# Kernel optimization log

Measured on AMD Instinct MI355X. Metric: run time of the kernel, lower is better.

Reference implementation:

```python
import jax, jax.numpy as jnp
import numpy as np

H = 8          # n_heads
M = 16         # max_dist
U = 512        # n_units
DH = U // H    # d_head
EPS = 1e-3     # keras LayerNormalization default epsilon
NEG = -2.0**32 + 1.0


def _rel_table(pe, T):
    # pe: [2M+1, DH]; returns [T, T, DH] with rel[i, j] = pe[clip(j - i, -M, M) + M]
    i = jnp.arange(T)
    idx = jnp.clip(i[None, :] - i[:, None], -M, M) + M
    return pe[idx]


def _split_heads(x):
    # [B, T, U] -> [H*B, T, DH]  (head-major, matching tf.concat(tf.split(x, H, 2), 0))
    B, T, _ = x.shape
    return x.reshape(B, T, H, DH).transpose(2, 0, 1, 3).reshape(H * B, T, DH)


def _merge_heads(x, B):
    # [H*B, T, DH] -> [B, T, U]
    T = x.shape[1]
    return x.reshape(H, B, T, DH).transpose(1, 2, 0, 3).reshape(B, T, U)


def setup_inputs() -> dict:
    key = jax.random.key(0)
    ks = jax.random.split(key, 10)
    B, T = 8, 1024
    s = 1.0 / np.sqrt(U)
    inp = {
        'q': jax.random.normal(ks[0], (B, T, U), jnp.float32),
        'k': jax.random.normal(ks[1], (B, T, U), jnp.float32),
        'v': jax.random.normal(ks[2], (B, T, U), jnp.float32),
        'Wq': jax.random.normal(ks[3], (U, U), jnp.float32) * s,
        'bq': jnp.zeros((U,), jnp.float32),
        'Wk': jax.random.normal(ks[4], (U, U), jnp.float32) * s,
        'bk': jnp.zeros((U,), jnp.float32),
        'Wv': jax.random.normal(ks[5], (U, U), jnp.float32) * s,
        'bv': jnp.zeros((U,), jnp.float32),
        'Wo': jax.random.normal(ks[6], (U, U), jnp.float32) * s,
        'bo': jnp.zeros((U,), jnp.float32),
        'gamma': jnp.ones((U,), jnp.float32),
        'beta': jnp.zeros((U,), jnp.float32),
        'pe_k': jax.random.normal(ks[7], (2 * M + 1, DH), jnp.float32) * 0.05,
        'pe_v': jax.random.normal(ks[8], (2 * M + 1, DH), jnp.float32) * 0.05,
    }
    return inp


def reference(q, k, v, Wq, bq, Wk, bk, Wv, bv, Wo, bo, gamma, beta, pe_k, pe_v):
    B, T, _ = q.shape
    relu = jax.nn.relu
    q_emb = relu(q @ Wq + bq)
    k_emb = relu(k @ Wk + bk)
    v_emb = relu(v @ Wv + bv)
    qh = _split_heads(q_emb)   # [HB, T, DH]
    kh = _split_heads(k_emb)
    vh = _split_heads(v_emb)

    attn = jnp.einsum('btd,bsd->bts', qh, kh)
    rel_k = _rel_table(pe_k, T)                       # [T, T, DH]
    attn = attn + jnp.einsum('btd,tsd->bts', qh, rel_k)
    attn = attn / jnp.asarray(DH, attn.dtype) ** 0.5

    causal = jnp.tril(jnp.ones((T, T), jnp.bool_))
    attn = jnp.where(causal[None], attn, jnp.asarray(NEG, attn.dtype))
    w = jax.nn.softmax(attn, axis=-1)

    out = jnp.einsum('bts,bsd->btd', w, vh)
    rel_v = _rel_table(pe_v, T)
    out = out + jnp.einsum('bts,tsd->btd', w, rel_v)

    out = _merge_heads(out, B)                        # [B, T, U]
    out = relu(out @ Wo + bo)
    out = out + q

    mu = jnp.mean(out, axis=-1, keepdims=True)
    var = jnp.mean(jnp.square(out - mu), axis=-1, keepdims=True)
    return (out - mu) * jax.lax.rsqrt(var + EPS) * gamma + beta
```

## Files before the change

### kernel.cpp

```cpp
#include <hip/hip_runtime.h>
#include <hip/hip_bf16.h>

#define T_SEQ 1024
#define U_DIM 512
#define LN_EPS 1e-3f
#define LOG2E 1.44269504f

typedef float  f32x4  __attribute__((ext_vector_type(4)));
typedef short  bf16x8 __attribute__((ext_vector_type(8)));

__device__ __forceinline__ unsigned short f2bf(float f) {
    union { float f; unsigned u; } x; x.f = f;
    unsigned r = x.u + 0x7fffu + ((x.u >> 16) & 1u);
    return (unsigned short)(r >> 16);
}
__device__ __forceinline__ float b2f(short s) {
    union { unsigned u; float f; } x; x.u = ((unsigned)(unsigned short)s) << 16;
    return x.f;
}
__device__ __forceinline__ int packbf(float a, float b) {
    return (int)((unsigned)f2bf(a) | ((unsigned)f2bf(b) << 16));
}
__device__ __forceinline__ void async_copy16(void* lds, const void* g) {
    __builtin_amdgcn_global_load_lds((const __attribute__((address_space(1))) void*)g,
                                     (__attribute__((address_space(3))) void*)lds, 16, 0, 0);
}

#define WAITV(N) asm volatile("s_waitcnt vmcnt(" #N ")" ::: "memory")

__global__ __launch_bounds__(256) void prep_wt(
        const float* __restrict__ Wq, const float* __restrict__ Wk,
        const float* __restrict__ Wv, const float* __restrict__ Wo,
        short* __restrict__ wt) {
    __shared__ float Ws[64][65];
    const int bid = blockIdx.x, t = threadIdx.x;
    const int z = bid >> 6, tile = bid & 63;
    const float* W = (z == 0) ? Wq : (z == 1) ? Wk : (z == 2) ? Wv : Wo;
    short* Wt = wt + (size_t)z * 262144;
    const int k0 = (tile >> 3) * 64, n0 = (tile & 7) * 64;
    {
        const int kr = t >> 2, cs = (t & 3) * 16;
        const float4* src = (const float4*)(W + (size_t)(k0 + kr) * 512 + n0 + cs);
#pragma unroll
        for (int i = 0; i < 4; ++i) {
            float4 vv = src[i];
            Ws[kr][cs + 4 * i + 0] = vv.x;
            Ws[kr][cs + 4 * i + 1] = vv.y;
            Ws[kr][cs + 4 * i + 2] = vv.z;
            Ws[kr][cs + 4 * i + 3] = vv.w;
        }
    }
    __syncthreads();
    {
        const int nr = t >> 2, ks = (t & 3) * 16;
        int4 w0, w1;
        w0.x = packbf(Ws[ks + 0][nr], Ws[ks + 1][nr]);
        w0.y = packbf(Ws[ks + 2][nr], Ws[ks + 3][nr]);
        w0.z = packbf(Ws[ks + 4][nr], Ws[ks + 5][nr]);
        w0.w = packbf(Ws[ks + 6][nr], Ws[ks + 7][nr]);
        w1.x = packbf(Ws[ks + 8][nr], Ws[ks + 9][nr]);
        w1.y = packbf(Ws[ks + 10][nr], Ws[ks + 11][nr]);
        w1.z = packbf(Ws[ks + 12][nr], Ws[ks + 13][nr]);
        w1.w = packbf(Ws[ks + 14][nr], Ws[ks + 15][nr]);
        short* dst = Wt + (size_t)(n0 + nr) * 512 + k0 + ks;
        *(int4*)dst = w0;
        *(int4*)(dst + 8) = w1;
    }
}

__global__ __launch_bounds__(256) void gemm_cvt(
        const float* __restrict__ A0, const float* __restrict__ A1, const float* __restrict__ A2,
        const short* __restrict__ Wt0, const short* __restrict__ Wt1, const short* __restrict__ Wt2,
        const float* __restrict__ b0p, const float* __restrict__ b1p, const float* __restrict__ b2p,
        short* __restrict__ O0, short* __restrict__ O1, short* __restrict__ O2) {
    __shared__ short As[2 * 8192];
    __shared__ short Bs[2 * 8192];

    const int z = blockIdx.z;
    const float* Av = (z == 0) ? A0 : (z == 1) ? A1 : A2;
    const short* Wz = (z == 0) ? Wt0 : (z == 1) ? Wt1 : Wt2;
    const float* bz = (z == 0) ? b0p : (z == 1) ? b1p : b2p;
    short* Ov = (z == 0) ? O0 : (z == 1) ? O1 : O2;

    const int tid = threadIdx.x;
    const int m0 = blockIdx.x * 128, n0 = blockIdx.y * 128;
    const int w = tid >> 6, lane = tid & 63;
    const int n15 = lane & 15, g = lane >> 4;
    const int mh = w >> 1, nh = w & 1;
    const int lr = tid >> 4, c4 = tid & 15;

    f32x4 acc[4][4];
#pragma unroll
    for (int i = 0; i < 4; ++i)
#pragma unroll
        for (int j = 0; j < 4; ++j) acc[i][j] = (f32x4){0.f, 0.f, 0.f, 0.f};

    float4 areg[8];

#define LOAD_A(CK)                                                                       \
    do {                                                                                 \
        const float* abase = Av + (size_t)(m0 + lr) * 512 + (CK) * 64 + c4 * 4;          \
        _Pragma("unroll")                                                                \
        for (int i = 0; i < 8; ++i) areg[i] = *(const float4*)(abase + (size_t)8192 * i); \
    } while (0)

#define STORE_A(BUF)                                                                     \
    do {                                                                                 \
        short* sb = As + (BUF) * 8192 + (c4 >> 3) * 8 * 512 + lr * 8 +                   \
                    ((c4 & 7) >> 1) * 128 + (c4 & 1) * 4;                                \
        _Pragma("unroll")                                                                \
        for (int i = 0; i < 8; ++i) {                                                    \
            int2 wv;                                                                     \
            wv.x = packbf(areg[i].x, areg[i].y);                                         \
            wv.y = packbf(areg[i].z, areg[i].w);                                         \
            *(int2*)(sb + i * 512) = wv;                                                 \
        }                                                                                \
    } while (0)

#define STAGE_B(CK, BUF)                                                                 \
    do {                                                                                 \
        if (w < 2) {                                                                     \
            _Pragma("unroll")                                                            \
            for (int i = 0; i < 8; ++i) {                                                \
                const int kc = i >> 2, nt = w * 4 + (i & 3);                             \
                const short* gp = Wz + (size_t)(n0 + nt * 16 + n15) * 512 + (CK) * 64 + kc * 32 + g * 8; \
                async_copy16(Bs + (BUF) * 8192 + (kc * 8 + nt) * 512, gp);               \
            }                                                                            \
        }                                                                                \
    } while (0)

    LOAD_A(0);
    STORE_A(0);
    STAGE_B(0, 0);
    LOAD_A(1);

    for (int ck = 0; ck < 8; ++ck) {
        const int cb = ck & 1, nb = cb ^ 1;
        __syncthreads();
        if (ck < 7) STAGE_B(ck + 1, nb);
#pragma unroll
        for (int kc = 0; kc < 2; ++kc) {
            bf16x8 af[4], bfv[4];
#pragma unroll
            for (int i = 0; i < 4; ++i)
                af[i] = *(const bf16x8*)(As + cb * 8192 + (kc * 8 + mh * 4 + i) * 512 + lane * 8);
#pragma unroll
            for (int j = 0; j < 4; ++j)
                bfv[j] = *(const bf16x8*)(Bs + cb * 8192 + (kc * 8 + nh * 4 + j) * 512 + lane * 8);
#pragma unroll
            for (int i = 0; i < 4; ++i)
#pragma unroll
                for (int j = 0; j < 4; ++j)
                    acc[i][j] = __builtin_amdgcn_mfma_f32_16x16x32_bf16(af[i], bfv[j], acc[i][j], 0, 0, 0);
        }
        if (ck < 7) {
            STORE_A(nb);
            if (ck < 6) LOAD_A(ck + 2);
        }
    }
#undef LOAD_A
#undef STORE_A
#undef STAGE_B

    const int mbase = m0 + mh * 64 + g * 4;
    const int nbase = n0 + nh * 64 + n15;
    const bool even = (n15 & 1) == 0;
    float bj[4];
#pragma unroll
    for (int j = 0; j < 4; ++j) bj[j] = bz[nbase + j * 16];

#pragma unroll
    for (int i = 0; i < 4; ++i) {
        const int mrow = mbase + i * 16;
#pragma unroll
        for (int j = 0; j < 4; ++j) {
            const int ncol = nbase + j * 16;
            f32x4 a = acc[i][j];
            float v0 = fmaxf(a[0] + bj[j], 0.f);
            float v1 = fmaxf(a[1] + bj[j], 0.f);
            float v2 = fmaxf(a[2] + bj[j], 0.f);
            float v3 = fmaxf(a[3] + bj[j], 0.f);
            unsigned t01 = (unsigned)packbf(v0, v1);
            unsigned t23 = (unsigned)packbf(v2, v3);
            unsigned x01 = (unsigned)__shfl_xor((int)t01, 1, 64);
            unsigned x23 = (unsigned)__shfl_xor((int)t23, 1, 64);
            if (even) {
                unsigned d0 = (t01 & 0xffffu) | (x01 << 16);
                unsigned d1 = (t01 >> 16) | (x01 & 0xffff0000u);
                *(unsigned*)(Ov + (size_t)(mrow + 0) * 512 + ncol) = d0;
                *(unsigned*)(Ov + (size_t)(mrow + 1) * 512 + ncol) = d1;
            } else {
                unsigned d2 = (x23 & 0xffffu) | (t23 << 16);
                unsigned d3 = (x23 >> 16) | (t23 & 0xffff0000u);
                *(unsigned*)(Ov + (size_t)(mrow + 2) * 512 + ncol - 1) = d2;
                *(unsigned*)(Ov + (size_t)(mrow + 3) * 512 + ncol - 1) = d3;
            }
        }
    }
}

template <int BM, int BN>
__global__ __launch_bounds__(256) void gemm_pipe(
        const short* __restrict__ Ab, const short* __restrict__ Wz,
        const float* __restrict__ bz, const float* __restrict__ resid,
        float* __restrict__ Oz) {
    constexpr int ASZ = BM * 32;
    constexpr int BSZ = BN * 32;
    constexpr int TSZ = ASZ + BSZ;
    constexpr int NA  = BM / 16;
    constexpr int NB  = BN / 16;
    constexpr int MW  = BM / 64;
    constexpr int NW  = 4 / MW;
    constexpr int AJ  = BN / (16 * NW);
    constexpr int LPW = (NA + NB) / 4;
    static_assert((NA + NB) % 4 == 0, "cells divisible by waves");
    __shared__ short Ls[4 * TSZ];

    const int tid = threadIdx.x;
    const int m0 = blockIdx.x * BM, n0 = blockIdx.y * BN;
    const int w = tid >> 6, lane = tid & 63;
    const int n15 = lane & 15, g = lane >> 4;
    const int mh = w / NW, nh = w % NW;

    f32x4 acc[4][AJ];
#pragma unroll
    for (int i = 0; i < 4; ++i)
#pragma unroll
        for (int j = 0; j < AJ; ++j) acc[i][j] = (f32x4){0.f, 0.f, 0.f, 0.f};

    const short* gsrc[LPW];
    int loff[LPW];
#pragma unroll
    for (int cl = 0; cl < LPW; ++cl) {
        const int cid = w * LPW + cl;
        if (cid < NA) {
            gsrc[cl] = Ab + (size_t)(m0 + cid * 16 + n15) * 512 + g * 8;
            loff[cl] = cid * 512;
        } else {
            const int c2 = cid - NA;
            gsrc[cl] = Wz + (size_t)(n0 + c2 * 16 + n15) * 512 + g * 8;
            loff[cl] = ASZ + c2 * 512;
        }
    }

#define STAGE(CK, BUF)                                                                   \
    do {                                                                                 \
        _Pragma("unroll")                                                                \
        for (int cl = 0; cl < LPW; ++cl)                                                 \
            async_copy16(Ls + (BUF) * TSZ + loff[cl], gsrc[cl] + (CK) * 32);             \
    } while (0)

    STAGE(0, 0);
    STAGE(1, 1);
    STAGE(2, 2);

    for (int ck = 0; ck < 16; ++ck) {
        if (ck < 14) {
            if constexpr (LPW == 3) WAITV(6); else WAITV(4);
        } else if (ck == 14) {
            if constexpr (LPW == 3) WAITV(3); else WAITV(2);
        } else {
            WAITV(0);
        }
        __builtin_amdgcn_s_barrier();
        __builtin_amdgcn_sched_barrier(0);
        if (ck + 3 <= 15) STAGE(ck + 3, (ck + 3) & 3);
        const int cb = ck & 3;
        bf16x8 af[4], bfv[AJ];
#pragma unroll
        for (int i = 0; i < 4; ++i)
            af[i] = *(const bf16x8*)(Ls + cb * TSZ + (mh * 4 + i) * 512 + lane * 8);
#pragma unroll
        for (int j = 0; j < AJ; ++j)
            bfv[j] = *(const bf16x8*)(Ls + cb * TSZ + ASZ + (nh * AJ + j) * 512 + lane * 8);
#pragma unroll
        for (int i = 0; i < 4; ++i)
#pragma unroll
            for (int j = 0; j < AJ; ++j)
                acc[i][j] = __builtin_amdgcn_mfma_f32_16x16x32_bf16(af[i], bfv[j], acc[i][j], 0, 0, 0);
    }
#undef STAGE

    const int mbase = m0 + mh * 64 + g * 4;
    const int nbase = n0 + nh * (AJ * 16) + n15;
    const bool even = (n15 & 1) == 0;
    float bj[AJ];
#pragma unroll
    for (int j = 0; j < AJ; ++j) bj[j] = bz[nbase + j * 16];

#pragma unroll
    for (int i = 0; i < 4; ++i) {
        const int mrow = mbase + i * 16;
#pragma unroll
        for (int j = 0; j < AJ; ++j) {
            const int ncol = nbase + j * 16;
            f32x4 a = acc[i][j];
            float v0 = fmaxf(a[0] + bj[j], 0.f);
            float v1 = fmaxf(a[1] + bj[j], 0.f);
            float v2 = fmaxf(a[2] + bj[j], 0.f);
            float v3 = fmaxf(a[3] + bj[j], 0.f);
            float x0 = __shfl_xor(v0, 1, 64);
            float x1 = __shfl_xor(v1, 1, 64);
            float x2 = __shfl_xor(v2, 1, 64);
            float x3 = __shfl_xor(v3, 1, 64);
            if (even) {
                float2 r0 = *(const float2*)(resid + (size_t)(mrow + 0) * 512 + ncol);
                float2 r1 = *(const float2*)(resid + (size_t)(mrow + 1) * 512 + ncol);
                *(float2*)(Oz + (size_t)(mrow + 0) * 512 + ncol) = make_float2(v0 + r0.x, x0 + r0.y);
                *(float2*)(Oz + (size_t)(mrow + 1) * 512 + ncol) = make_float2(v1 + r1.x, x1 + r1.y);
            } else {
                float2 r2 = *(const float2*)(resid + (size_t)(mrow + 2) * 512 + ncol - 1);
                float2 r3 = *(const float2*)(resid + (size_t)(mrow + 3) * 512 + ncol - 1);
                *(float2*)(Oz + (size_t)(mrow + 2) * 512 + ncol - 1) = make_float2(x2 + r2.x, v2 + r2.y);
                *(float2*)(Oz + (size_t)(mrow + 3) * 512 + ncol - 1) = make_float2(x3 + r3.x, v3 + r3.y);
            }
        }
    }
}

__global__ __launch_bounds__(256, 4) void attn_mfma(
        const short* __restrict__ qe, const short* __restrict__ ke,
        const short* __restrict__ ve, const float* __restrict__ pe_k,
        float* __restrict__ ml, float* __restrict__ ml1, float* __restrict__ ml2,
        short* __restrict__ ao, short* __restrict__ ao2) {
    __shared__ short Kc[4096];
    __shared__ short Vc[4096];
    __shared__ float qpeS[4 * 16 * 17];

    static const unsigned char tbl[24] = {
        7, 22, 6, 4, 3, 1,
        20, 23, 16, 12, 9, 0,
        18, 5, 14, 15, 17, 2,
        19, 21, 8, 10, 11, 13
    };

    const int tid = threadIdx.x;
    const int r6 = blockIdx.x >> 8, c = blockIdx.x & 255;
    const int hb = c >> 2, q4 = c & 3;
    const int slot = tbl[q4 * 6 + r6];
    int tt, g0, g1, mode;
    if (slot < 8) {
        tt = slot; g0 = 0; g1 = slot + 1; mode = 0;
    } else {
        const int i2 = (slot - 8) >> 1;
        tt = 8 + i2;
        const int n = tt + 1, hh = (n + 1) >> 1;
        if (((slot - 8) & 1) == 0) { g0 = 0; g1 = hh; mode = 1; }
        else                       { g0 = hh; g1 = n; mode = 2; }
    }
    const int h = hb >> 3, b = hb & 7;
    const int w = tid >> 6, lane = tid & 63;
    const int g = lane >> 4, n15 = lane & 15;
    const int sp = tid & 31, dbase = (tid >> 5) * 8;
    float* qpeW = qpeS + w * (16 * 17);

    const size_t rowbase = (size_t)b * T_SEQ;
    short* aoP = (mode == 2) ? ao2 : ao;
    float* mlP = (mode == 0) ? ml : (mode == 1 ? ml1 : ml2);

    const int qn = tt * 64 + w * 16;
    bf16x8 Bq[2];
    float qpe0 = 0.f;
    float m_r = -1.0e38f, l_r = 0.f, m2 = -1.4427e38f;
    f32x4 oacc[4];

    {
#pragma unroll
        for (int kh = 0; kh < 2; ++kh) {
            bf16x8 t = *(const bf16x8*)(qe + (rowbase + qn + n15) * U_DIM + h * 64 + kh * 32 + g * 8);
#pragma unroll
            for (int i2 = 0; i2 < 8; ++i2) {
                unsigned short u = (unsigned short)t[i2];
                t[i2] = (short)(((u & 0x7f80u) > 0x0180u) ? (unsigned short)(u - 0x0180u)
                                                          : (unsigned short)(u & 0x8000u));
            }
            Bq[kh] = t;
        }
        f32x4 qa[2];
        qa[0] = (f32x4){0.f, 0.f, 0.f, 0.f};
        qa[1] = (f32x4){0.f, 0.f, 0.f, 0.f};
#pragma unroll
        for (int mt = 0; mt < 2; ++mt)
#pragma unroll
        for (int kh = 0; kh < 2; ++kh) {
            const float* src = pe_k + (mt * 16 + n15) * 64 + kh * 32 + g * 8;
            float4 f0 = *(const float4*)src;
            float4 f1 = *(const float4*)(src + 4);
            bf16x8 fr;
            fr[0] = (short)f2bf(f0.x); fr[1] = (short)f2bf(f0.y);
            fr[2] = (short)f2bf(f0.z); fr[3] = (short)f2bf(f0.w);
            fr[4] = (short)f2bf(f1.x); fr[5] = (short)f2bf(f1.y);
            fr[6] = (short)f2bf(f1.z); fr[7] = (short)f2bf(f1.w);
            qa[mt] = __builtin_amdgcn_mfma_f32_16x16x32_bf16(fr, Bq[kh], qa[mt], 0, 0, 0);
        }
#pragma unroll
        for (int mt = 0; mt < 2; ++mt)
#pragma unroll
        for (int r = 0; r < 4; ++r) {
            const int ri = mt * 16 + 4 * g + r;
            if (ri <= 16) qpeW[n15 * 17 + ri] = qa[mt][r];
        }
        qpe0 = qpeW[n15 * 17];
#pragma unroll
        for (int dt = 0; dt < 4; ++dt) oacc[dt] = (f32x4){0.f, 0.f, 0.f, 0.f};
    }

    const int sK = tid >> 2, dK = (tid & 3) * 16;
    short* kdst = Kc + (((tid & 3) >> 1) * 4 + (tid >> 6)) * 512 +
                  ((sK & 15) + 16 * ((tid & 1) * 2)) * 8;

#define LOAD_K(S)                                                                        \
    do {                                                                                 \
        const short* kp = ke + (rowbase + (S) + sK) * U_DIM + h * 64 + dK;               \
        kx0 = *(const bf16x8*)kp;                                                        \
        kx1 = *(const bf16x8*)(kp + 8);                                                  \
    } while (0)

#define STORE_K()                                                                        \
    do {                                                                                 \
        *(bf16x8*)kdst = kx0;                                                            \
        *(bf16x8*)(kdst + 128) = kx1;                                                    \
    } while (0)

#define LOAD_V(S)                                                                        \
    do {                                                                                 \
        const short* r0 = ve + (rowbase + (S) + 2 * sp) * U_DIM + h * 64 + dbase;        \
        vx = *(const bf16x8*)r0;                                                        \
        vy = *(const bf16x8*)(r0 + U_DIM);                                              \
    } while (0)

#define STORE_V()                                                                        \
    do {                                                                                 \
        const int vkh = sp >> 4, vg = (sp & 15) >> 2, vj = (sp & 3) * 2;                 \
        _Pragma("unroll")                                                                \
        for (int i = 0; i < 8; ++i) {                                                    \
            const int d = dbase + i;                                                     \
            int pv = (int)((unsigned short)vx[i]) | (((int)(unsigned short)vy[i]) << 16);\
            *(int*)(Vc + (vkh * 4 + (d >> 4)) * 512 + ((d & 15) + 16 * vg) * 8 + vj) = pv; \
        }                                                                                \
    } while (0)

    bf16x8 kx0, kx1, vx, vy;
    LOAD_K(g0 * 64);
    LOAD_V(g0 * 64);

    for (int gs = g0; gs < g1; ++gs) {
        const int s0 = gs * 64;
        __syncthreads();
        STORE_K();
        STORE_V();
        __syncthreads();
        if (gs + 1 < g1) {
            LOAD_K((gs + 1) * 64);
            LOAD_V((gs + 1) * 64);
        }

        {
            int cls[4];
#pragma unroll
            for (int mt = 0; mt < 4; ++mt) {
                const int slo = s0 + mt * 16;
                cls[mt] = (slo > qn + 15) ? 0 : ((slo + 31 < qn) ? 1 : 2);
            }
            f32x4 cc2[4];
#pragma unroll
            for (int mt = 0; mt < 4; ++mt) cc2[mt] = (f32x4){0.f, 0.f, 0.f, 0.f};
            __builtin_amdgcn_s_setprio(1);
#pragma unroll
            for (int mt = 0; mt < 4; ++mt) {
                if (!cls[mt]) continue;
#pragma unroll
                for (int kh = 0; kh < 2; ++kh) {
                    bf16x8 ak = *(const bf16x8*)(Kc + (kh * 4 + mt) * 512 + lane * 8);
                    cc2[mt] = __builtin_amdgcn_mfma_f32_16x16x32_bf16(ak, Bq[kh], cc2[mt], 0, 0, 0);
                }
            }
            __builtin_amdgcn_s_setprio(0);

            const int qg = qn + n15;
            float sc[4][4];
            float pmax = -3.0e38f;
#pragma unroll
            for (int mt = 0; mt < 4; ++mt) {
                if (cls[mt] == 0) {
#pragma unroll
                    for (int r = 0; r < 4; ++r) sc[mt][r] = -3.0e38f;
                } else if (cls[mt] == 1) {
#pragma unroll
                    for (int r = 0; r < 4; ++r) {
                        sc[mt][r] = cc2[mt][r] + qpe0;
                        pmax = fmaxf(pmax, sc[mt][r]);
                    }
                } else {
#pragma unroll
                    for (int r = 0; r < 4; ++r) {
                        const int sg = s0 + mt * 16 + 4 * g + r;
                        const int dlt = sg - qg;
                        if (dlt <= 0) {
                            const int ri = (dlt < -16) ? 0 : (dlt + 16);
                            sc[mt][r] = cc2[mt][r] + qpeW[n15 * 17 + ri];
                            pmax = fmaxf(pmax, sc[mt][r]);
                        } else {
                            sc[mt][r] = -3.0e38f;
                        }
                    }
                }
            }
            pmax = fmaxf(pmax, __shfl_xor(pmax, 16, 64));
            pmax = fmaxf(pmax, __shfl_xor(pmax, 32, 64));

            const bool resc = __any(pmax > m_r + 8.0f);
            float alpha = 1.0f;
            if (resc) {
                const float mnew = fmaxf(m_r, pmax);
                alpha = __expf(m_r - mnew);
                m_r = mnew;
                m2 = mnew * LOG2E;
            }
            float p[4][4];
            float psum = 0.f;
#pragma unroll
            for (int mt = 0; mt < 4; ++mt)
#pragma unroll
            for (int r = 0; r < 4; ++r) {
                const float pv = (cls[mt] == 0) ? 0.f
                                : exp2f(fmaf(sc[mt][r], LOG2E, -m2));
                p[mt][r] = pv;
                psum += pv;
            }
            psum += __shfl_xor(psum, 16, 64);
            psum += __shfl_xor(psum, 32, 64);
            l_r = l_r * alpha + psum;

            int pk01[4], pk23[4];
#pragma unroll
            for (int mt = 0; mt < 4; ++mt) {
                asm("v_cvt_pk_bf16_f32 %0, %1, %2" : "=v"(pk01[mt]) : "v"(p[mt][0]), "v"(p[mt][1]));
                asm("v_cvt_pk_bf16_f32 %0, %1, %2" : "=v"(pk23[mt]) : "v"(p[mt][2]), "v"(p[mt][3]));
            }
            const int srcA = ((g & 1) * 2) * 16 + n15;
            const int srcB = srcA + 16;
            const bool selHi = (g >> 1) != 0;
            if (resc) {
                float aO[4];
#pragma unroll
                for (int r = 0; r < 4; ++r) aO[r] = __shfl(alpha, 4 * g + r, 64);
#pragma unroll
                for (int dt = 0; dt < 4; ++dt)
#pragma unroll
                for (int r = 0; r < 4; ++r) oacc[dt][r] *= aO[r];
            }
#pragma unroll
            for (int kh = 0; kh < 2; ++kh) {
                if (cls[2 * kh] == 0 && cls[2 * kh + 1] == 0) continue;
                const int a0l = __shfl(pk01[2 * kh], srcA, 64);
                const int a0h = __shfl(pk01[2 * kh + 1], srcA, 64);
                const int a1l = __shfl(pk23[2 * kh], srcA, 64);
                const int a1h = __shfl(pk23[2 * kh + 1], srcA, 64);
                const int a2l = __shfl(pk01[2 * kh], srcB, 64);
                const int a2h = __shfl(pk01[2 * kh + 1], srcB, 64);
                const int a3l = __shfl(pk23[2 * kh], srcB, 64);
                const int a3h = __shfl(pk23[2 * kh + 1], srcB, 64);
                union { int i[4]; bf16x8 v; } au;
                au.i[0] = selHi ? a0h : a0l;
                au.i[1] = selHi ? a1h : a1l;
                au.i[2] = selHi ? a2h : a2l;
                au.i[3] = selHi ? a3h : a3l;
                __builtin_amdgcn_s_setprio(1);
#pragma unroll
                for (int dt = 0; dt < 4; ++dt) {
                    bf16x8 bv = *(const bf16x8*)(Vc + (kh * 4 + dt) * 512 + lane * 8);
                    oacc[dt] = __builtin_amdgcn_mfma_f32_16x16x32_bf16(au.v, bv, oacc[dt], 0, 0, 0);
                }
                __builtin_amdgcn_s_setprio(0);
            }
        }
    }

    if (g == 0)
        *(float2*)(mlP + ((size_t)hb * T_SEQ + qn + n15) * 2) = make_float2(m_r, l_r);
#pragma unroll
    for (int r = 0; r < 4; ++r) {
        const float lq = __shfl(l_r, 4 * g + r, 64);
        const float linv = (lq > 0.f) ? 1.0f / lq : 0.f;
        short* dst = aoP + (rowbase + qn + 4 * g + r) * U_DIM + h * 64 + n15;
#pragma unroll
        for (int dt = 0; dt < 4; ++dt)
            dst[dt * 16] = (short)f2bf(oacc[dt][r] * linv);
    }
#undef LOAD_K
#undef STORE_K
#undef LOAD_V
#undef STORE_V
}

__global__ __launch_bounds__(256) void attn_combine(
        const float* __restrict__ ml1, const float* __restrict__ ml2,
        const short* __restrict__ ao2, short* __restrict__ ao,
        float* __restrict__ ml) {
    const int bid = blockIdx.x;
    const int hb = bid >> 3;
    const int t = 512 + ((bid & 7) << 6) + (threadIdx.x >> 2);
    const int R = hb * 1024 + t;
    const int h = hb >> 3, b = hb & 7;
    const int d0 = (threadIdx.x & 3) * 16;
    const float2 p1 = *(const float2*)(ml1 + (size_t)R * 2);
    const float2 p2 = *(const float2*)(ml2 + (size_t)R * 2);
    const float m = fmaxf(p1.x, p2.x);
    const float w1 = p1.y * __expf(p1.x - m);
    const float w2 = (p2.y > 0.f) ? p2.y * __expf(p2.x - m) : 0.f;
    const float inv = 1.0f / (w1 + w2);
    const float a1 = w1 * inv, a2 = w2 * inv;
    const size_t off = (size_t)(b * T_SEQ + t) * U_DIM + h * 64 + d0;
    short* op = ao + off;
    const short* o2p = ao2 + off;
    bf16x8 x0 = *(const bf16x8*)op, x1 = *(const bf16x8*)(op + 8);
    bf16x8 y0 = *(const bf16x8*)o2p, y1 = *(const bf16x8*)(o2p + 8);
    const bool has2 = (w2 > 0.f);
    float o[16];
#pragma unroll
    for (int i = 0; i < 8; ++i) {
        float t0 = a1 * b2f(x0[i]);
        float t1 = a1 * b2f(x1[i]);
        o[i]     = has2 ? (t0 + a2 * b2f(y0[i])) : t0;
        o[8 + i] = has2 ? (t1 + a2 * b2f(y1[i])) : t1;
    }
    int4 o0, o1;
    o0.x = packbf(o[0], o[1]);   o0.y = packbf(o[2], o[3]);
    o0.z = packbf(o[4], o[5]);   o0.w = packbf(o[6], o[7]);
    o1.x = packbf(o[8], o[9]);   o1.y = packbf(o[10], o[11]);
    o1.z = packbf(o[12], o[13]); o1.w = packbf(o[14], o[15]);
    *(int4*)op = o0;
    *(int4*)(op + 8) = o1;
    if ((threadIdx.x & 3) == 0)
        *(float2*)(ml + (size_t)R * 2) = make_float2(m, w1 + w2);
}

__global__ __launch_bounds__(256) void band_relv(
        const short* __restrict__ qe, const short* __restrict__ ke,
        const float* __restrict__ pe_k, const float* __restrict__ pe_v,
        const float* __restrict__ ml, short* __restrict__ ao) {
    __shared__ float pek[17 * 64];
    __shared__ float pev[17 * 64];
    const int tb = blockIdx.x, hb = blockIdx.y;
    const int h = hb >> 3, b = hb & 7;
    const int tid = threadIdx.x;
    for (int i = tid; i < 17 * 64; i += 256) {
        pek[i] = b2f((short)f2bf(pe_k[i]));
        pev[i] = pe_v[i];
    }
    __syncthreads();

    const int t = tb * 64 + (tid >> 2);
    const int p = (tid & 3) * 16;
    const short* qp = qe + (size_t)(b * T_SEQ + t) * U_DIM + h * 64 + p;
    bf16x8 qa = *(const bf16x8*)qp, qb2 = *(const bf16x8*)(qp + 8);
    float qv[16];
#pragma unroll
    for (int i = 0; i < 8; ++i) { qv[i] = b2f(qa[i]); qv[8 + i] = b2f(qb2[i]); }

    float dots[17];
#pragma unroll
    for (int ri = 0; ri < 17; ++ri) {
        const int s = t - 16 + ri;
        float acc = 0.f;
        if (s >= 0) {
            const short* kp = ke + (size_t)(b * T_SEQ + s) * U_DIM + h * 64 + p;
            bf16x8 ka = *(const bf16x8*)kp, kb2 = *(const bf16x8*)(kp + 8);
#pragma unroll
            for (int d = 0; d < 8; ++d) {
                acc += qv[d] * b2f(ka[d]);
                acc += qv[8 + d] * b2f(kb2[d]);
            }
#pragma unroll
            for (int d = 0; d < 16; ++d) acc += qv[d] * pek[ri * 64 + p + d];
        }
        dots[ri] = acc;
    }
#pragma unroll
    for (int ri = 0; ri < 17; ++ri) {
        dots[ri] += __shfl_xor(dots[ri], 1, 64);
        dots[ri] += __shfl_xor(dots[ri], 2, 64);
    }

    const float2 mlv = *(const float2*)(ml + ((size_t)hb * T_SEQ + t) * 2);
    const float m = mlv.x, linv = 1.0f / mlv.y;
    float wv[17];
    float wsum = 0.f;
#pragma unroll
    for (int ri = 0; ri < 17; ++ri) {
        const int s = t - 16 + ri;
        const float wr = (s >= 0) ? __expf(dots[ri] * 0.125f - m) * linv : 0.f;
        wv[ri] = wr;
        wsum += wr;
    }
    wv[0] += 1.0f - wsum;

    float relv[16];
#pragma unroll
    for (int d = 0; d < 16; ++d) relv[d] = 0.f;
#pragma unroll
    for (int ri = 0; ri < 17; ++ri)
#pragma unroll
        for (int d = 0; d < 16; ++d) relv[d] += wv[ri] * pev[ri * 64 + p + d];

    short* op = ao + (size_t)(b * T_SEQ + t) * U_DIM + h * 64 + p;
    bf16x8 a0 = *(const bf16x8*)op, a1 = *(const bf16x8*)(op + 8);
    int4 o0, o1;
    o0.x = packbf(b2f(a0[0]) + relv[0],  b2f(a0[1]) + relv[1]);
    o0.y = packbf(b2f(a0[2]) + relv[2],  b2f(a0[3]) + relv[3]);
    o0.z = packbf(b2f(a0[4]) + relv[4],  b2f(a0[5]) + relv[5]);
    o0.w = packbf(b2f(a0[6]) + relv[6],  b2f(a0[7]) + relv[7]);
    o1.x = packbf(b2f(a1[0]) + relv[8],  b2f(a1[1]) + relv[9]);
    o1.y = packbf(b2f(a1[2]) + relv[10], b2f(a1[3]) + relv[11]);
    o1.z = packbf(b2f(a1[4]) + relv[12], b2f(a1[5]) + relv[13]);
    o1.w = packbf(b2f(a1[6]) + relv[14], b2f(a1[7]) + relv[15]);
    *(int4*)op = o0;
    *(int4*)(op + 8) = o1;
}

__global__ __launch_bounds__(256) void ln_kernel(float* __restrict__ io,
                                                 const float* __restrict__ gamma,
                                                 const float* __restrict__ beta) {
    const int row = blockIdx.x * 4 + (threadIdx.x >> 6);
    const int lane = threadIdx.x & 63;
    float* rp = io + (size_t)row * 512 + lane * 8;
    float4 a = *(const float4*)rp;
    float4 c = *(const float4*)(rp + 4);
    float v[8] = {a.x, a.y, a.z, a.w, c.x, c.y, c.z, c.w};

    float s = v[0] + v[1] + v[2] + v[3] + v[4] + v[5] + v[6] + v[7];
#pragma unroll
    for (int off = 1; off < 64; off <<= 1) s += __shfl_xor(s, off, 64);
    const float mu = s * (1.0f / 512.0f);

    float sq = 0.f;
#pragma unroll
    for (int i = 0; i < 8; ++i) { v[i] -= mu; sq += v[i] * v[i]; }
#pragma unroll
    for (int off = 1; off < 64; off <<= 1) sq += __shfl_xor(sq, off, 64);
    const float rs = rsqrtf(sq * (1.0f / 512.0f) + LN_EPS);

    const float4 g0 = *(const float4*)(gamma + lane * 8);
    const float4 g1 = *(const float4*)(gamma + lane * 8 + 4);
    const float4 b0 = *(const float4*)(beta + lane * 8);
    const float4 b1 = *(const float4*)(beta + lane * 8 + 4);
    float4 o0, o1;
    o0.x = v[0] * rs * g0.x + b0.x;
    o0.y = v[1] * rs * g0.y + b0.y;
    o0.z = v[2] * rs * g0.z + b0.z;
    o0.w = v[3] * rs * g0.w + b0.w;
    o1.x = v[4] * rs * g1.x + b1.x;
    o1.y = v[5] * rs * g1.y + b1.y;
    o1.z = v[6] * rs * g1.z + b1.z;
    o1.w = v[7] * rs * g1.w + b1.w;
    *(float4*)rp = o0;
    *(float4*)(rp + 4) = o1;
}

extern "C" void kernel_launch(void* const* d_in, const int* in_sizes, int n_in,
                              void* d_out, int out_size, void* d_ws, size_t ws_size,
                              hipStream_t stream) {
    const float* q     = (const float*)d_in[0];
    const float* k     = (const float*)d_in[1];
    const float* v     = (const float*)d_in[2];
    const float* Wq    = (const float*)d_in[3];
    const float* bq    = (const float*)d_in[4];
    const float* Wk    = (const float*)d_in[5];
    const float* bk    = (const float*)d_in[6];
    const float* Wv    = (const float*)d_in[7];
    const float* bv    = (const float*)d_in[8];
    const float* Wo    = (const float*)d_in[9];
    const float* bo    = (const float*)d_in[10];
    const float* gamma = (const float*)d_in[11];
    const float* beta  = (const float*)d_in[12];
    const float* pe_k  = (const float*)d_in[13];
    const float* pe_v  = (const float*)d_in[14];
    float* out = (float*)d_out;

    char* base = (char*)d_ws;
    short* qe = (short*)(base);
    short* ke = (short*)(base + (((size_t)8) << 20));
    short* ve = (short*)(base + (((size_t)16) << 20));
    short* ao = (short*)(base + (((size_t)24) << 20));
    short* wt = (short*)(base + (((size_t)32) << 20));
    float* ml = (float*)(base + (((size_t)34) << 20));
    float* ml1 = (float*)(base + (((size_t)35) << 20));
    short* ao2 = (short*)(base + (((size_t)36) << 20));
    float* ml2 = (float*)(base + (((size_t)44) << 20));
    short* wtq = wt, *wtk = wt + 262144, *wtv = wt + 2 * 262144, *wto = wt + 3 * 262144;

    prep_wt<<<dim3(256), 256, 0, stream>>>(Wq, Wk, Wv, Wo, wt);
    gemm_cvt<<<dim3(64, 4, 3), 256, 0, stream>>>(
        q, k, v, wtq, wtk, wtv, bq, bk, bv, qe, ke, ve);
    attn_mfma<<<dim3(1536), 256, 0, stream>>>(qe, ke, ve, pe_k, ml, ml1, ml2, ao, ao2);
    attn_combine<<<dim3(512), 256, 0, stream>>>(ml1, ml2, ao2, ao, ml);
    band_relv<<<dim3(16, 64), 256, 0, stream>>>(qe, ke, pe_k, pe_v, ml, ao);
    gemm_pipe<64, 128><<<dim3(128, 4), 256, 0, stream>>>(ao, wto, bo, q, out);
    ln_kernel<<<dim3(2048), 256, 0, stream>>>(out, gamma, beta);
}
```

Baseline: 242.9 us.

## Double-buffer K/V tiles with async LDS copies and fuse split-combine into band_relv

The attention kernel now double-buffers the K and V tiles in LDS. K is staged with direct global-to-LDS async copies, and V is stored into the next buffer after the compute, which removes one barrier per iteration. The separate attn_combine kernel is folded into band_relv, which merges the two split-softmax partials before adding the relative-value term. This saves a launch and one read/write pass over the attention output. In exchange, LDS use per block doubles, which may reduce occupancy at four blocks per CU, and the K layout now depends on the async copy addressing matching the MFMA fragment layout.

```diff
diff --git a/kernel.cpp b/kernel.cpp
--- a/kernel.cpp
+++ b/kernel.cpp
@@ -323,8 +323,8 @@
         const short* __restrict__ ve, const float* __restrict__ pe_k,
         float* __restrict__ ml, float* __restrict__ ml1, float* __restrict__ ml2,
         short* __restrict__ ao, short* __restrict__ ao2) {
-    __shared__ short Kc[4096];
-    __shared__ short Vc[4096];
+    __shared__ short Kc[2 * 4096];
+    __shared__ short Vc[2 * 4096];
     __shared__ float qpeS[4 * 16 * 17];
 
     static const unsigned char tbl[24] = {
@@ -405,21 +405,14 @@
         for (int dt = 0; dt < 4; ++dt) oacc[dt] = (f32x4){0.f, 0.f, 0.f, 0.f};
     }
 
-    const int sK = tid >> 2, dK = (tid & 3) * 16;
-    short* kdst = Kc + (((tid & 3) >> 1) * 4 + (tid >> 6)) * 512 +
-                  ((sK & 15) + 16 * ((tid & 1) * 2)) * 8;
-
-#define LOAD_K(S)                                                                        \
+#define STAGE_K(S, BUF)                                                                  \
     do {                                                                                 \
-        const short* kp = ke + (rowbase + (S) + sK) * U_DIM + h * 64 + dK;               \
-        kx0 = *(const bf16x8*)kp;                                                        \
-        kx1 = *(const bf16x8*)(kp + 8);                                                  \
-    } while (0)
-
-#define STORE_K()                                                                        \
-    do {                                                                                 \
-        *(bf16x8*)kdst = kx0;                                                            \
-        *(bf16x8*)(kdst + 128) = kx1;                                                    \
+        _Pragma("unroll")                                                                \
+        for (int j = 0; j < 2; ++j) {                                                    \
+            const int cc = w * 2 + j, kh = cc >> 2, mt = cc & 3;                         \
+            const short* gp = ke + (rowbase + (S) + mt * 16 + n15) * U_DIM + h * 64 + kh * 32 + g * 8; \
+            async_copy16(Kc + (BUF) * 4096 + cc * 512, gp);                              \
+        }                                                                                \
     } while (0)
 
 #define LOAD_V(S)                                                                        \
@@ -429,29 +422,29 @@
         vy = *(const bf16x8*)(r0 + U_DIM);                                              \
     } while (0)
 
-#define STORE_V()                                                                        \
+#define STORE_V(BUF)                                                                     \
     do {                                                                                 \
         const int vkh = sp >> 4, vg = (sp & 15) >> 2, vj = (sp & 3) * 2;                 \
         _Pragma("unroll")                                                                \
         for (int i = 0; i < 8; ++i) {                                                    \
             const int d = dbase + i;                                                     \
             int pv = (int)((unsigned short)vx[i]) | (((int)(unsigned short)vy[i]) << 16);\
-            *(int*)(Vc + (vkh * 4 + (d >> 4)) * 512 + ((d & 15) + 16 * vg) * 8 + vj) = pv; \
+            *(int*)(Vc + (BUF) * 4096 + (vkh * 4 + (d >> 4)) * 512 + ((d & 15) + 16 * vg) * 8 + vj) = pv; \
         }                                                                                \
     } while (0)
 
-    bf16x8 kx0, kx1, vx, vy;
-    LOAD_K(g0 * 64);
+    bf16x8 vx, vy;
+    STAGE_K(g0 * 64, 0);
     LOAD_V(g0 * 64);
+    STORE_V(0);
 
     for (int gs = g0; gs < g1; ++gs) {
+        const int ls = gs - g0;
+        const int cb = ls & 1, nb = cb ^ 1;
         const int s0 = gs * 64;
         __syncthreads();
-        STORE_K();
-        STORE_V();
-        __syncthreads();
         if (gs + 1 < g1) {
-            LOAD_K((gs + 1) * 64);
+            STAGE_K((gs + 1) * 64, nb);
             LOAD_V((gs + 1) * 64);
         }
 
@@ -471,7 +464,7 @@
                 if (!cls[mt]) continue;
 #pragma unroll
                 for (int kh = 0; kh < 2; ++kh) {
-                    bf16x8 ak = *(const bf16x8*)(Kc + (kh * 4 + mt) * 512 + lane * 8);
+                    bf16x8 ak = *(const bf16x8*)(Kc + cb * 4096 + (kh * 4 + mt) * 512 + lane * 8);
                     cc2[mt] = __builtin_amdgcn_mfma_f32_16x16x32_bf16(ak, Bq[kh], cc2[mt], 0, 0, 0);
                 }
             }
@@ -569,12 +562,14 @@
                 __builtin_amdgcn_s_setprio(1);
 #pragma unroll
                 for (int dt = 0; dt < 4; ++dt) {
-                    bf16x8 bv = *(const bf16x8*)(Vc + (kh * 4 + dt) * 512 + lane * 8);
+                    bf16x8 bv = *(const bf16x8*)(Vc + cb * 4096 + (kh * 4 + dt) * 512 + lane * 8);
                     oacc[dt] = __builtin_amdgcn_mfma_f32_16x16x32_bf16(au.v, bv, oacc[dt], 0, 0, 0);
                 }
                 __builtin_amdgcn_s_setprio(0);
             }
         }
+
+        if (gs + 1 < g1) STORE_V(nb);
     }
 
     if (g == 0)
@@ -588,58 +583,17 @@
         for (int dt = 0; dt < 4; ++dt)
             dst[dt * 16] = (short)f2bf(oacc[dt][r] * linv);
     }
-#undef LOAD_K
-#undef STORE_K
+#undef STAGE_K
 #undef LOAD_V
 #undef STORE_V
-}
-
-__global__ __launch_bounds__(256) void attn_combine(
-        const float* __restrict__ ml1, const float* __restrict__ ml2,
-        const short* __restrict__ ao2, short* __restrict__ ao,
-        float* __restrict__ ml) {
-    const int bid = blockIdx.x;
-    const int hb = bid >> 3;
-    const int t = 512 + ((bid & 7) << 6) + (threadIdx.x >> 2);
-    const int R = hb * 1024 + t;
-    const int h = hb >> 3, b = hb & 7;
-    const int d0 = (threadIdx.x & 3) * 16;
-    const float2 p1 = *(const float2*)(ml1 + (size_t)R * 2);
-    const float2 p2 = *(const float2*)(ml2 + (size_t)R * 2);
-    const float m = fmaxf(p1.x, p2.x);
-    const float w1 = p1.y * __expf(p1.x - m);
-    const float w2 = (p2.y > 0.f) ? p2.y * __expf(p2.x - m) : 0.f;
-    const float inv = 1.0f / (w1 + w2);
-    const float a1 = w1 * inv, a2 = w2 * inv;
-    const size_t off = (size_t)(b * T_SEQ + t) * U_DIM + h * 64 + d0;
-    short* op = ao + off;
-    const short* o2p = ao2 + off;
-    bf16x8 x0 = *(const bf16x8*)op, x1 = *(const bf16x8*)(op + 8);
-    bf16x8 y0 = *(const bf16x8*)o2p, y1 = *(const bf16x8*)(o2p + 8);
-    const bool has2 = (w2 > 0.f);
-    float o[16];
-#pragma unroll
-    for (int i = 0; i < 8; ++i) {
-        float t0 = a1 * b2f(x0[i]);
-        float t1 = a1 * b2f(x1[i]);
-        o[i]     = has2 ? (t0 + a2 * b2f(y0[i])) : t0;
-        o[8 + i] = has2 ? (t1 + a2 * b2f(y1[i])) : t1;
-    }
-    int4 o0, o1;
-    o0.x = packbf(o[0], o[1]);   o0.y = packbf(o[2], o[3]);
-    o0.z = packbf(o[4], o[5]);   o0.w = packbf(o[6], o[7]);
-    o1.x = packbf(o[8], o[9]);   o1.y = packbf(o[10], o[11]);
-    o1.z = packbf(o[12], o[13]); o1.w = packbf(o[14], o[15]);
-    *(int4*)op = o0;
-    *(int4*)(op + 8) = o1;
-    if ((threadIdx.x & 3) == 0)
-        *(float2*)(ml + (size_t)R * 2) = make_float2(m, w1 + w2);
 }
 
 __global__ __launch_bounds__(256) void band_relv(
         const short* __restrict__ qe, const short* __restrict__ ke,
         const float* __restrict__ pe_k, const float* __restrict__ pe_v,
-        const float* __restrict__ ml, short* __restrict__ ao) {
+        const float* __restrict__ ml, const float* __restrict__ ml1,
+        const float* __restrict__ ml2, const short* __restrict__ ao2,
+        short* __restrict__ ao) {
     __shared__ float pek[17 * 64];
     __shared__ float pev[17 * 64];
     const int tb = blockIdx.x, hb = blockIdx.y;
@@ -653,6 +607,7 @@
 
     const int t = tb * 64 + (tid >> 2);
     const int p = (tid & 3) * 16;
+    const int R = hb * 1024 + t;
     const short* qp = qe + (size_t)(b * T_SEQ + t) * U_DIM + h * 64 + p;
     bf16x8 qa = *(const bf16x8*)qp, qb2 = *(const bf16x8*)(qp + 8);
     float qv[16];
@@ -683,8 +638,39 @@
         dots[ri] += __shfl_xor(dots[ri], 2, 64);
     }
 
-    const float2 mlv = *(const float2*)(ml + ((size_t)hb * T_SEQ + t) * 2);
-    const float m = mlv.x, linv = 1.0f / mlv.y;
+    const size_t off = (size_t)(b * T_SEQ + t) * U_DIM + h * 64 + p;
+    short* op = ao + off;
+    float m, l;
+    float o[16];
+    if (tb >= 8) {
+        const float2 p1 = *(const float2*)(ml1 + (size_t)R * 2);
+        const float2 p2 = *(const float2*)(ml2 + (size_t)R * 2);
+        m = fmaxf(p1.x, p2.x);
+        const float w1 = (p1.y > 0.f) ? p1.y * __expf(p1.x - m) : 0.f;
+        const float w2 = (p2.y > 0.f) ? p2.y * __expf(p2.x - m) : 0.f;
+        l = w1 + w2;
+        const float inv = 1.0f / l;
+        const float a1 = w1 * inv, a2 = w2 * inv;
+        bf16x8 x0 = *(const bf16x8*)op, x1 = *(const bf16x8*)(op + 8);
+        const short* o2p = ao2 + off;
+        bf16x8 y0 = *(const bf16x8*)o2p, y1 = *(const bf16x8*)(o2p + 8);
+#pragma unroll
+        for (int i = 0; i < 8; ++i) {
+            o[i]     = a1 * b2f(x0[i]) + a2 * b2f(y0[i]);
+            o[8 + i] = a1 * b2f(x1[i]) + a2 * b2f(y1[i]);
+        }
+    } else {
+        const float2 mlv = *(const float2*)(ml + (size_t)R * 2);
+        m = mlv.x; l = mlv.y;
+        bf16x8 x0 = *(const bf16x8*)op, x1 = *(const bf16x8*)(op + 8);
+#pragma unroll
+        for (int i = 0; i < 8; ++i) {
+            o[i]     = b2f(x0[i]);
+            o[8 + i] = b2f(x1[i]);
+        }
+    }
+    const float linv = 1.0f / l;
+
     float wv[17];
     float wsum = 0.f;
 #pragma unroll
@@ -704,17 +690,15 @@
 #pragma unroll
         for (int d = 0; d < 16; ++d) relv[d] += wv[ri] * pev[ri * 64 + p + d];
 
-    short* op = ao + (size_t)(b * T_SEQ + t) * U_DIM + h * 64 + p;
-    bf16x8 a0 = *(const bf16x8*)op, a1 = *(const bf16x8*)(op + 8);
     int4 o0, o1;
-    o0.x = packbf(b2f(a0[0]) + relv[0],  b2f(a0[1]) + relv[1]);
-    o0.y = packbf(b2f(a0[2]) + relv[2],  b2f(a0[3]) + relv[3]);
-    o0.z = packbf(b2f(a0[4]) + relv[4],  b2f(a0[5]) + relv[5]);
-    o0.w = packbf(b2f(a0[6]) + relv[6],  b2f(a0[7]) + relv[7]);
-    o1.x = packbf(b2f(a1[0]) + relv[8],  b2f(a1[1]) + relv[9]);
-    o1.y = packbf(b2f(a1[2]) + relv[10], b2f(a1[3]) + relv[11]);
-    o1.z = packbf(b2f(a1[4]) + relv[12], b2f(a1[5]) + relv[13]);
-    o1.w = packbf(b2f(a1[6]) + relv[14], b2f(a1[7]) + relv[15]);
+    o0.x = packbf(o[0] + relv[0],   o[1] + relv[1]);
+    o0.y = packbf(o[2] + relv[2],   o[3] + relv[3]);
+    o0.z = packbf(o[4] + relv[4],   o[5] + relv[5]);
+    o0.w = packbf(o[6] + relv[6],   o[7] + relv[7]);
+    o1.x = packbf(o[8] + relv[8],   o[9] + relv[9]);
+    o1.y = packbf(o[10] + relv[10], o[11] + relv[11]);
+    o1.z = packbf(o[12] + relv[12], o[13] + relv[13]);
+    o1.w = packbf(o[14] + relv[14], o[15] + relv[15]);
     *(int4*)op = o0;
     *(int4*)(op + 8) = o1;
 }
@@ -794,8 +778,7 @@
     gemm_cvt<<<dim3(64, 4, 3), 256, 0, stream>>>(
         q, k, v, wtq, wtk, wtv, bq, bk, bv, qe, ke, ve);
     attn_mfma<<<dim3(1536), 256, 0, stream>>>(qe, ke, ve, pe_k, ml, ml1, ml2, ao, ao2);
-    attn_combine<<<dim3(512), 256, 0, stream>>>(ml1, ml2, ao2, ao, ml);
-    band_relv<<<dim3(16, 64), 256, 0, stream>>>(qe, ke, pe_k, pe_v, ml, ao);
+    band_relv<<<dim3(16, 64), 256, 0, stream>>>(qe, ke, pe_k, pe_v, ml, ml1, ml2, ao2, ao);
     gemm_pipe<64, 128><<<dim3(128, 4), 256, 0, stream>>>(ao, wto, bo, q, out);
     ln_kernel<<<dim3(2048), 256, 0, stream>>>(out, gamma, beta);
 }
```

Result: no change. 246.6 us (+1.5%).
